# Kernel optimization log

Measured on AMD Instinct MI355X. Metric: run time of the kernel, lower is better.

The kernel has to match this reference:

```python
import jax, jax.numpy as jnp
import numpy as np

B, S, D, H, L = 32, 512, 512, 8, 6
NQ, FF, V, C = 8, 2048, 32000, 10
DK = D // H
EPS = 1e-5


def _layernorm(x, g, b):
    mu = jnp.mean(x, axis=-1, keepdims=True)
    var = jnp.mean(jnp.square(x - mu), axis=-1, keepdims=True)
    return (x - mu) * jax.lax.rsqrt(var + EPS) * g + b


def _pos_encoding(seq_len, dim):
    pos = jnp.arange(seq_len, dtype=jnp.float32)[:, None]
    div = jnp.exp(jnp.arange(0, dim, 2, dtype=jnp.float32) * (-jnp.log(10000.0) / dim))
    pe = jnp.zeros((seq_len, dim), dtype=jnp.float32)
    pe = pe.at[:, 0::2].set(jnp.sin(pos * div))
    pe = pe.at[:, 1::2].set(jnp.cos(pos * div))
    return pe


def setup_inputs() -> dict:
    key = jax.random.key(0)
    ks = jax.random.split(key, 16)
    sd = 0.02
    return {
        "x": jax.random.randint(ks[0], (B, S), 0, V),
        "emb": jax.random.normal(ks[1], (V, D), jnp.float32) * sd,
        "ln1_g": jnp.ones((L, D), jnp.float32),
        "ln1_b": jnp.zeros((L, D), jnp.float32),
        "ln2_g": jnp.ones((L, D), jnp.float32),
        "ln2_b": jnp.zeros((L, D), jnp.float32),
        "attn_w": jax.random.normal(ks[2], (L, D, D), jnp.float32) * sd,
        "attn_b": jnp.zeros((L, D), jnp.float32),
        "theta": jax.random.normal(ks[3], (L, NQ), jnp.float32),
        "ffn_w1": jax.random.normal(ks[4], (L, NQ, FF), jnp.float32) * sd,
        "ffn_b1": jnp.zeros((L, FF), jnp.float32),
        "ffn_w2": jax.random.normal(ks[5], (L, FF, D), jnp.float32) * sd,
        "ffn_b2": jnp.zeros((L, D), jnp.float32),
        "clf_w": jax.random.normal(ks[6], (D, C), jnp.float32) * sd,
        "clf_b": jnp.zeros((C,), jnp.float32),
    }


def reference(x, emb, ln1_g, ln1_b, ln2_g, ln2_b, attn_w, attn_b, theta,
              ffn_w1, ffn_b1, ffn_w2, ffn_b2, clf_w, clf_b):
    h = emb[x] + _pos_encoding(S, D)[None]  # [B,S,D]
    scale = 1.0 / jnp.sqrt(jnp.float32(DK))
    for l in range(L):
        # --- MultiHeadAttentionQuantum: q=k=v=reshape(x), no projections ---
        q = h.reshape(B, S, H, DK)
        scores = jnp.einsum('bihd,bjhd->bhij', q, q) * scale
        p = jax.nn.softmax(scores, axis=-1)
        attn = jnp.einsum('bhij,bjhd->bihd', p, q).reshape(B, S, D)
        attn = attn @ attn_w[l] + attn_b[l]
        h = _layernorm(h + attn, ln1_g[l], ln1_b[l])
        # --- FeedForwardQuantum: per-wire RX-encode -> RY(theta) -> <Z> = cos(x)cos(theta) ---
        qout = jnp.cos(h[..., :NQ]) * jnp.cos(theta[l])  # [B,S,NQ]
        f = jax.nn.relu(qout @ ffn_w1[l] + ffn_b1[l]) @ ffn_w2[l] + ffn_b2[l]
        h = _layernorm(h + f, ln2_g[l], ln2_b[l])
    pooled = jnp.mean(h, axis=1)  # [B,D]
    return pooled @ clf_w + clf_b  # [B,C]
```

## Files before the change

### kernel.cpp

```cpp
#include <hip/hip_runtime.h>
#include <hip/hip_bf16.h>
#include <math.h>

#define BB 32
#define SS 512
#define DD 512
#define HH 8
#define DK 64
#define LL 6
#define NQ 8
#define FF 2048
#define CC 10

typedef unsigned int uint;
typedef unsigned short ushort_t;
using bf16x8 = __attribute__((ext_vector_type(8))) short;
using f32x4  = __attribute__((ext_vector_type(4))) float;

#define MFMA(a, b, c) __builtin_amdgcn_mfma_f32_16x16x32_bf16((a), (b), (c), 0, 0, 0)

union U8 { ushort_t u[8]; bf16x8 v; };

__device__ __forceinline__ void gload16(const void* g, void* l) {
    __builtin_amdgcn_global_load_lds((__attribute__((address_space(1))) void*)g,
                                     (__attribute__((address_space(3))) void*)l,
                                     16, 0, 0);
}

__device__ inline ushort_t f2bf(float x) {
    uint u = __float_as_uint(x);
    u += 0x7FFFu + ((u >> 16) & 1u);
    return (ushort_t)(u >> 16);
}
__device__ inline void tsplit(float v, ushort_t& hi, ushort_t& lo) {
    uint u = __float_as_uint(v);
    hi = (ushort_t)(u >> 16);
    lo = f2bf(v - __uint_as_float(u & 0xFFFF0000u));
}
__device__ inline void tsplit_fast(float v, ushort_t& hi, ushort_t& lo) {
    uint u = __float_as_uint(v);
    hi = (ushort_t)(u >> 16);
    float res = v - __uint_as_float(u & 0xFFFF0000u);
    lo = (ushort_t)(__float_as_uint(res) >> 16);
}
__device__ inline uint packsplit(float v) {
    uint u = __float_as_uint(v) & 0xFFFF0000u;
    uint ru = __float_as_uint(v - __uint_as_float(u));
    ru += 0x7FFFu + ((ru >> 16) & 1u);
    return u | (ru >> 16);
}
__device__ inline float unpackf(uint u) {
    return __uint_as_float(u & 0xFFFF0000u) + __uint_as_float(u << 16);
}

__global__ __launch_bounds__(256) void embed_pe(const int* __restrict__ x,
                                                const float* __restrict__ emb,
                                                uint* __restrict__ Hp) {
    int idx = blockIdx.x * 256 + threadIdx.x;
    if (idx >= BB * SS * DD) return;
    int d = idx & (DD - 1);
    int s = (idx >> 9) & (SS - 1);
    int tok = x[idx >> 9];
    int i2 = d >> 1;
    float freq = expf((float)(2 * i2) * (-9.210340371976184f / (float)DD));
    float ang = (float)s * freq;
    float pe = (d & 1) ? cosf(ang) : sinf(ang);
    Hp[idx] = packsplit(emb[(size_t)tok * DD + d] + pe);
}

__global__ __launch_bounds__(256) void transpose_split_w(const float* __restrict__ in,
                                                         ushort_t* __restrict__ outh,
                                                         ushort_t* __restrict__ outl,
                                                         int K, int N) {
    __shared__ ushort_t th[64][68], tl[64][68];
    int nb = N >> 6;
    int k0 = ((int)blockIdx.x / nb) << 6;
    int n0 = ((int)blockIdx.x % nb) << 6;
    int t = threadIdx.x;
    int r = t >> 2, cb = (t & 3) << 4;
#pragma unroll
    for (int c = 0; c < 4; c++) {
        float4 v = *reinterpret_cast<const float4*>(&in[(size_t)(k0 + r) * N + n0 + cb + 4 * c]);
        float vv[4] = {v.x, v.y, v.z, v.w};
#pragma unroll
        for (int e = 0; e < 4; e++) {
            ushort_t hb, lb; tsplit(vv[e], hb, lb);
            th[r][cb + 4 * c + e] = hb;
            tl[r][cb + 4 * c + e] = lb;
        }
    }
    __syncthreads();
    int n = t >> 2, kb = (t & 3) << 4;
#pragma unroll
    for (int c = 0; c < 4; c++) {
        ushort4 oh, ol;
        oh.x = th[kb + 4 * c + 0][n]; ol.x = tl[kb + 4 * c + 0][n];
        oh.y = th[kb + 4 * c + 1][n]; ol.y = tl[kb + 4 * c + 1][n];
        oh.z = th[kb + 4 * c + 2][n]; ol.z = tl[kb + 4 * c + 2][n];
        oh.w = th[kb + 4 * c + 3][n]; ol.w = tl[kb + 4 * c + 3][n];
        *reinterpret_cast<ushort4*>(&outh[(size_t)(n0 + n) * K + k0 + kb + 4 * c]) = oh;
        *reinterpret_cast<ushort4*>(&outl[(size_t)(n0 + n) * K + k0 + kb + 4 * c]) = ol;
    }
}

__global__ __launch_bounds__(256) void prep_w1t(const float* __restrict__ W1all,
                                                ushort_t* __restrict__ outh,
                                                ushort_t* __restrict__ outl) {
    int l = blockIdx.y;
    int f = blockIdx.x * 256 + threadIdx.x;
    const float* W1 = W1all + (size_t)l * NQ * FF;
    U8 ph, pl;
#pragma unroll
    for (int n = 0; n < 8; n++) {
        ushort_t hb, lb; tsplit(W1[n * FF + f], hb, lb);
        ph.u[n] = hb; pl.u[n] = lb;
    }
    *reinterpret_cast<bf16x8*>(&outh[((size_t)l * FF + f) * 8]) = ph.v;
    *reinterpret_cast<bf16x8*>(&outl[((size_t)l * FF + f) * 8]) = pl.v;
}

__global__ __launch_bounds__(512, 4) void flash_attn_split(const uint* __restrict__ Hp,
                                                           ushort_t* __restrict__ outh,
                                                           ushort_t* __restrict__ outl) {
    __shared__ __align__(16) ushort_t Kh[64][72], Kl[64][72];
    __shared__ __align__(16) ushort_t Vh[64][72], Vl[64][72];
    __shared__ __align__(16) ushort_t Ph[128][72], Pl[128][72];

    int i0 = blockIdx.x * 128;
    int h0 = blockIdx.y * DK;
    int b  = blockIdx.z;
    const uint* baseH = Hp + (size_t)b * (SS * DD);

    int t = threadIdx.x;
    int w = t >> 6;
    int ln = t & 63;
    int l15 = ln & 15, lh = ln >> 4;

    bf16x8 aqh0, aqh1, aql0, aql1;
    {
        int row = i0 + w * 16 + l15;
        const uint* src = &baseH[(size_t)row * DD + h0 + lh * 8];
        uint4 p0 = *reinterpret_cast<const uint4*>(src);
        uint4 p1 = *reinterpret_cast<const uint4*>(src + 4);
        uint4 p2 = *reinterpret_cast<const uint4*>(src + 32);
        uint4 p3 = *reinterpret_cast<const uint4*>(src + 36);
        uint a0[8] = {p0.x, p0.y, p0.z, p0.w, p1.x, p1.y, p1.z, p1.w};
        uint a1[8] = {p2.x, p2.y, p2.z, p2.w, p3.x, p3.y, p3.z, p3.w};
        U8 h0u, l0u, h1u, l1u;
#pragma unroll
        for (int e = 0; e < 8; e++) {
            h0u.u[e] = (ushort_t)(a0[e] >> 16);
            l0u.u[e] = (ushort_t)(a0[e] & 0xFFFFu);
            h1u.u[e] = (ushort_t)(a1[e] >> 16);
            l1u.u[e] = (ushort_t)(a1[e] & 0xFFFFu);
        }
        aqh0 = h0u.v; aql0 = l0u.v; aqh1 = h1u.v; aql1 = l1u.v;
    }

    float m_[4], l_[4], al[4];
    f32x4 acc[4];
    f32x4 z4 = {0.f, 0.f, 0.f, 0.f};
#pragma unroll
    for (int r = 0; r < 4; r++) { m_[r] = -1e30f; l_[r] = 0.f; acc[r] = z4; }

    int kr = t >> 3, kcb = (t & 7) * 8;
    int vc = t & 7, vr = t >> 3;

    for (int j0 = 0; j0 < SS; j0 += 64) {
        __syncthreads();
        {
            const uint* src = &baseH[(size_t)(j0 + kr) * DD + h0 + kcb];
            uint4 p0 = *reinterpret_cast<const uint4*>(src);
            uint4 p1 = *reinterpret_cast<const uint4*>(src + 4);
            uint a[8] = {p0.x, p0.y, p0.z, p0.w, p1.x, p1.y, p1.z, p1.w};
            U8 kh, kl;
#pragma unroll
            for (int e = 0; e < 8; e++) {
                kh.u[e] = (ushort_t)(a[e] >> 16);
                kl.u[e] = (ushort_t)(a[e] & 0xFFFFu);
            }
            *reinterpret_cast<bf16x8*>(&Kh[kr][kcb]) = kh.v;
            *reinterpret_cast<bf16x8*>(&Kl[kr][kcb]) = kl.v;
        }
        __syncthreads();
#pragma unroll
        for (int e = 0; e < 8; e++) {
            int d = vc + 8 * e;
            Vh[d][vr] = Kh[vr][d];
            Vl[d][vr] = Kl[vr][d];
        }
        f32x4 sc[4];
#pragma unroll
        for (int tt = 0; tt < 4; tt++) {
            bf16x8 bh0 = *reinterpret_cast<const bf16x8*>(&Kh[tt * 16 + l15][lh * 8]);
            bf16x8 bh1 = *reinterpret_cast<const bf16x8*>(&Kh[tt * 16 + l15][32 + lh * 8]);
            bf16x8 bl0 = *reinterpret_cast<const bf16x8*>(&Kl[tt * 16 + l15][lh * 8]);
            bf16x8 bl1 = *reinterpret_cast<const bf16x8*>(&Kl[tt * 16 + l15][32 + lh * 8]);
            f32x4 s = z4;
            s = MFMA(aqh0, bh0, s);
            s = MFMA(aqh1, bh1, s);
            s = MFMA(aqh0, bl0, s);
            s = MFMA(aqh1, bl1, s);
            s = MFMA(aql0, bh0, s);
            s = MFMA(aql1, bh1, s);
            sc[tt] = s * 0.125f;
        }
#pragma unroll
        for (int r = 0; r < 4; r++) {
            float mx = fmaxf(fmaxf(sc[0][r], sc[1][r]), fmaxf(sc[2][r], sc[3][r]));
            mx = fmaxf(mx, __shfl_xor(mx, 1));
            mx = fmaxf(mx, __shfl_xor(mx, 2));
            mx = fmaxf(mx, __shfl_xor(mx, 4));
            mx = fmaxf(mx, __shfl_xor(mx, 8));
            float nm = fmaxf(m_[r], mx);
            al[r] = __expf(m_[r] - nm);
            m_[r] = nm;
            float rs = 0.f;
#pragma unroll
            for (int tt = 0; tt < 4; tt++) {
                float p = __expf(sc[tt][r] - nm);
                sc[tt][r] = p;
                rs += p;
            }
            rs += __shfl_xor(rs, 1);
            rs += __shfl_xor(rs, 2);
            rs += __shfl_xor(rs, 4);
            rs += __shfl_xor(rs, 8);
            l_[r] = l_[r] * al[r] + rs;
        }
#pragma unroll
        for (int tt = 0; tt < 4; tt++)
#pragma unroll
            for (int r = 0; r < 4; r++) {
                ushort_t hb, lb; tsplit(sc[tt][r], hb, lb);
                Ph[w * 16 + lh * 4 + r][tt * 16 + l15] = hb;
                Pl[w * 16 + lh * 4 + r][tt * 16 + l15] = lb;
            }
        __syncthreads();
#pragma unroll
        for (int td = 0; td < 4; td++) {
            acc[td][0] *= al[0];
            acc[td][1] *= al[1];
            acc[td][2] *= al[2];
            acc[td][3] *= al[3];
        }
        bf16x8 aph0 = *reinterpret_cast<const bf16x8*>(&Ph[w * 16 + l15][lh * 8]);
        bf16x8 aph1 = *reinterpret_cast<const bf16x8*>(&Ph[w * 16 + l15][32 + lh * 8]);
        bf16x8 apl0 = *reinterpret_cast<const bf16x8*>(&Pl[w * 16 + l15][lh * 8]);
        bf16x8 apl1 = *reinterpret_cast<const bf16x8*>(&Pl[w * 16 + l15][32 + lh * 8]);
#pragma unroll
        for (int td = 0; td < 4; td++) {
            bf16x8 bvh0 = *reinterpret_cast<const bf16x8*>(&Vh[td * 16 + l15][lh * 8]);
            bf16x8 bvh1 = *reinterpret_cast<const bf16x8*>(&Vh[td * 16 + l15][32 + lh * 8]);
            bf16x8 bvl0 = *reinterpret_cast<const bf16x8*>(&Vl[td * 16 + l15][lh * 8]);
            bf16x8 bvl1 = *reinterpret_cast<const bf16x8*>(&Vl[td * 16 + l15][32 + lh * 8]);
            acc[td] = MFMA(aph0, bvh0, acc[td]);
            acc[td] = MFMA(aph1, bvh1, acc[td]);
            acc[td] = MFMA(aph0, bvl0, acc[td]);
            acc[td] = MFMA(aph1, bvl1, acc[td]);
            acc[td] = MFMA(apl0, bvh0, acc[td]);
            acc[td] = MFMA(apl1, bvh1, acc[td]);
        }
    }

#pragma unroll
    for (int r = 0; r < 4; r++) {
        float inv = 1.f / l_[r];
        int row = i0 + w * 16 + lh * 4 + r;
#pragma unroll
        for (int td = 0; td < 4; td++) {
            float o = acc[td][r] * inv;
            ushort_t hb, lb; tsplit(o, hb, lb);
            size_t idx = (size_t)b * SS * DD + (size_t)row * DD + h0 + td * 16 + l15;
            outh[idx] = hb;
            outl[idx] = lb;
        }
    }
}

#define SWZREAD(plane, row, ks) \
    (*reinterpret_cast<const bf16x8*>(&(plane)[row][((((ks) * 4 + lh) ^ ((row) & 7)) * 8)]))

__global__ __launch_bounds__(512, 2) void gemm_split(const ushort_t* __restrict__ Ah,
                                                     const ushort_t* __restrict__ Al,
                                                     const ushort_t* __restrict__ Bth,
                                                     const ushort_t* __restrict__ Btl,
                                                     const float* __restrict__ bias,
                                                     float* __restrict__ C,
                                                     int M, int N, int K) {
    __shared__ __align__(16) ushort_t sAh[2][128][64], sAl[2][128][64];
    __shared__ __align__(16) ushort_t sBh[2][128][64], sBl[2][128][64];
    int nb = N >> 7;
    int m0 = ((int)blockIdx.x / nb) << 7;
    int n0 = ((int)blockIdx.x % nb) << 7;
    int t = threadIdx.x;
    int w = t >> 6, ln = t & 63, l15 = ln & 15, lh = ln >> 4;
    int wr = (w >> 2) * 64, wc = (w & 3) * 32;

    f32x4 z4 = {0.f, 0.f, 0.f, 0.f};
    f32x4 acc[4][2];
#pragma unroll
    for (int i = 0; i < 4; i++)
#pragma unroll
        for (int j = 0; j < 2; j++) acc[i][j] = z4;

    int srow = ln >> 3;
    int schunk = (ln & 7) ^ srow;

    auto stage = [&](int buf, int kk) {
#pragma unroll
        for (int p = 0; p < 2; p++) {
            int rbase = (w + p * 8) * 8;
            int grow = rbase + srow;
            int gc = kk + schunk * 8;
            gload16(&Ah[(size_t)(m0 + grow) * K + gc],  &sAh[buf][rbase][0]);
            gload16(&Al[(size_t)(m0 + grow) * K + gc],  &sAl[buf][rbase][0]);
            gload16(&Bth[(size_t)(n0 + grow) * K + gc], &sBh[buf][rbase][0]);
            gload16(&Btl[(size_t)(n0 + grow) * K + gc], &sBl[buf][rbase][0]);
        }
    };

    stage(0, 0);
    __syncthreads();
    int cur = 0;
    int ntile = K >> 6;

    for (int kt = 0; kt < ntile; kt++) {
        if (kt + 1 < ntile) stage(cur ^ 1, (kt + 1) * 64);
#pragma unroll
        for (int ks = 0; ks < 2; ks++) {
            bf16x8 ah[4], al_[4];
#pragma unroll
            for (int mt = 0; mt < 4; mt++) {
                int row = wr + mt * 16 + l15;
                ah[mt]  = SWZREAD(sAh[cur], row, ks);
                al_[mt] = SWZREAD(sAl[cur], row, ks);
            }
#pragma unroll
            for (int nt = 0; nt < 2; nt++) {
                int row = wc + nt * 16 + l15;
                bf16x8 bh = SWZREAD(sBh[cur], row, ks);
                bf16x8 bl = SWZREAD(sBl[cur], row, ks);
#pragma unroll
                for (int mt = 0; mt < 4; mt++) {
                    acc[mt][nt] = MFMA(ah[mt], bh, acc[mt][nt]);
                    acc[mt][nt] = MFMA(ah[mt], bl, acc[mt][nt]);
                    acc[mt][nt] = MFMA(al_[mt], bh, acc[mt][nt]);
                }
            }
        }
        __syncthreads();
        cur ^= 1;
    }
#pragma unroll
    for (int nt = 0; nt < 2; nt++) {
        int col = n0 + wc + nt * 16 + l15;
        float bs = bias[col];
#pragma unroll
        for (int mt = 0; mt < 4; mt++)
#pragma unroll
            for (int r = 0; r < 4; r++)
                C[(size_t)(m0 + wr + mt * 16 + lh * 4 + r) * N + col] = acc[mt][nt][r] + bs;
    }
}

__global__ __launch_bounds__(256) void ln_residual(uint* __restrict__ Hp,
                                                   const float* __restrict__ add,
                                                   const float* __restrict__ g,
                                                   const float* __restrict__ bta) {
    int row = blockIdx.x * 4 + (threadIdx.x >> 6);
    int lane = threadIdx.x & 63;
    uint* hp = Hp + (size_t)row * DD;
    const float* ap = add + (size_t)row * DD;
    float v[8];
    float sum = 0.f;
#pragma unroll
    for (int i = 0; i < 8; i++) {
        int d = lane + i * 64;
        v[i] = unpackf(hp[d]) + ap[d];
        sum += v[i];
    }
#pragma unroll
    for (int off = 32; off > 0; off >>= 1) sum += __shfl_xor(sum, off);
    float mu = sum * (1.f / DD);
    float s2 = 0.f;
#pragma unroll
    for (int i = 0; i < 8; i++) {
        float d2 = v[i] - mu;
        s2 += d2 * d2;
    }
#pragma unroll
    for (int off = 32; off > 0; off >>= 1) s2 += __shfl_xor(s2, off);
    float inv = rsqrtf(s2 * (1.f / DD) + 1e-5f);
#pragma unroll
    for (int i = 0; i < 8; i++) {
        int d = lane + i * 64;
        hp[d] = packsplit((v[i] - mu) * inv * g[d] + bta[d]);
    }
}

__global__ __launch_bounds__(512, 2) void ffn_split(const uint* __restrict__ Hp,
                                                    const ushort_t* __restrict__ W1th,
                                                    const ushort_t* __restrict__ W1tl,
                                                    const float* __restrict__ b1,
                                                    const ushort_t* __restrict__ W2th,
                                                    const ushort_t* __restrict__ W2tl,
                                                    const float* __restrict__ b2,
                                                    const float* __restrict__ theta,
                                                    float* __restrict__ outp) {
    __shared__ __align__(16) ushort_t Abh[128][72], Abl[128][72];
    __shared__ __align__(16) ushort_t sBh[2][128][64], sBl[2][128][64];
    __shared__ __align__(16) ushort_t qsh[129][8], qsl[129][8];
    __shared__ float tcs[8];

    int t = threadIdx.x;
    int m0 = (int)(blockIdx.x >> 2) * 128;
    int n0 = (int)(blockIdx.x & 3) * 128;
    if (t < 8) {
        tcs[t] = cosf(theta[t]);
        qsh[128][t] = 0;
        qsl[128][t] = 0;
    }
    __syncthreads();
#pragma unroll
    for (int i = 0; i < 2; i++) {
        int idx = t + i * 512;
        int m = idx >> 3, n = idx & 7;
        float q = cosf(unpackf(Hp[(size_t)(m0 + m) * DD + n])) * tcs[n];
        ushort_t hb, lb; tsplit(q, hb, lb);
        qsh[m][n] = hb;
        qsl[m][n] = lb;
    }

    int w = t >> 6, ln = t & 63, l15 = ln & 15, lh = ln >> 4;
    int wr = (w >> 2) * 64, wc = (w & 3) * 32;
    bool lh0 = (lh == 0);
    f32x4 z4 = {0.f, 0.f, 0.f, 0.f};
    bf16x8 z8 = {0, 0, 0, 0, 0, 0, 0, 0};
    f32x4 acc[4][2];
#pragma unroll
    for (int i = 0; i < 4; i++)
#pragma unroll
        for (int j = 0; j < 2; j++) acc[i][j] = z4;

    int srow = ln >> 3;
    int schunk = (ln & 7) ^ srow;

    auto stageB = [&](int buf, int kk) {
#pragma unroll
        for (int p = 0; p < 2; p++) {
            int rbase = (w + p * 8) * 8;
            int grow = rbase + srow;
            int gc = kk + schunk * 8;
            gload16(&W2th[(size_t)(n0 + grow) * FF + gc], &sBh[buf][rbase][0]);
            gload16(&W2tl[(size_t)(n0 + grow) * FF + gc], &sBl[buf][rbase][0]);
        }
    };

    bf16x8 rwh[4], rwl[4];
    stageB(0, 0);
#pragma unroll
    for (int fq = 0; fq < 4; fq++) {
        rwh[fq] = *reinterpret_cast<const bf16x8*>(&W1th[(size_t)(fq * 16 + l15) * 8]);
        rwl[fq] = *reinterpret_cast<const bf16x8*>(&W1tl[(size_t)(fq * 16 + l15) * 8]);
    }
    __syncthreads();
    int cur = 0;

    for (int k0 = 0; k0 < FF; k0 += 64) {
        {
            bf16x8 wh[4], wl[4];
#pragma unroll
            for (int fq = 0; fq < 4; fq++) {
                wh[fq] = lh0 ? rwh[fq] : z8;
                wl[fq] = lh0 ? rwl[fq] : z8;
            }
            int m = w * 16 + l15;
            int mrow = lh0 ? m : 128;
            bf16x8 qh  = *reinterpret_cast<const bf16x8*>(&qsh[mrow][0]);
            bf16x8 ql_ = *reinterpret_cast<const bf16x8*>(&qsl[mrow][0]);
#pragma unroll
            for (int fq = 0; fq < 4; fq++) {
                f32x4 d = z4;
                d = MFMA(wh[fq], qh, d);
                d = MFMA(wh[fq], ql_, d);
                d = MFMA(wl[fq], qh, d);
                float4 b1v = *reinterpret_cast<const float4*>(&b1[k0 + fq * 16 + lh * 4]);
                float v0 = fmaxf(d[0] + b1v.x, 0.f);
                float v1 = fmaxf(d[1] + b1v.y, 0.f);
                float v2 = fmaxf(d[2] + b1v.z, 0.f);
                float v3 = fmaxf(d[3] + b1v.w, 0.f);
                ushort_t h0_, l0_, h1_, l1_, h2_, l2_, h3_, l3_;
                tsplit_fast(v0, h0_, l0_);
                tsplit_fast(v1, h1_, l1_);
                tsplit_fast(v2, h2_, l2_);
                tsplit_fast(v3, h3_, l3_);
                uint2 hu, lu;
                hu.x = (uint)h0_ | ((uint)h1_ << 16);
                hu.y = (uint)h2_ | ((uint)h3_ << 16);
                lu.x = (uint)l0_ | ((uint)l1_ << 16);
                lu.y = (uint)l2_ | ((uint)l3_ << 16);
                *reinterpret_cast<uint2*>(&Abh[m][fq * 16 + lh * 4]) = hu;
                *reinterpret_cast<uint2*>(&Abl[m][fq * 16 + lh * 4]) = lu;
            }
        }
        __syncthreads();
        if (k0 + 64 < FF) {
            int k1 = k0 + 64;
            stageB(cur ^ 1, k1);
#pragma unroll
            for (int fq = 0; fq < 4; fq++) {
                rwh[fq] = *reinterpret_cast<const bf16x8*>(&W1th[(size_t)(k1 + fq * 16 + l15) * 8]);
                rwl[fq] = *reinterpret_cast<const bf16x8*>(&W1tl[(size_t)(k1 + fq * 16 + l15) * 8]);
            }
        }
#pragma unroll
        for (int ks = 0; ks < 2; ks++) {
            bf16x8 ah[4], al_[4];
#pragma unroll
            for (int mt = 0; mt < 4; mt++) {
                ah[mt]  = *reinterpret_cast<const bf16x8*>(&Abh[wr + mt * 16 + l15][ks * 32 + lh * 8]);
                al_[mt] = *reinterpret_cast<const bf16x8*>(&Abl[wr + mt * 16 + l15][ks * 32 + lh * 8]);
            }
#pragma unroll
            for (int nt = 0; nt < 2; nt++) {
                int row = wc + nt * 16 + l15;
                bf16x8 bh = SWZREAD(sBh[cur], row, ks);
                bf16x8 bl = SWZREAD(sBl[cur], row, ks);
#pragma unroll
                for (int mt = 0; mt < 4; mt++) {
                    acc[mt][nt] = MFMA(ah[mt], bh, acc[mt][nt]);
                    acc[mt][nt] = MFMA(ah[mt], bl, acc[mt][nt]);
                    acc[mt][nt] = MFMA(al_[mt], bh, acc[mt][nt]);
                }
            }
        }
        __syncthreads();
        cur ^= 1;
    }
#pragma unroll
    for (int nt = 0; nt < 2; nt++) {
        int col = n0 + wc + nt * 16 + l15;
        float bs = b2[col];
#pragma unroll
        for (int mt = 0; mt < 4; mt++)
#pragma unroll
            for (int r = 0; r < 4; r++)
                outp[(size_t)(m0 + wr + mt * 16 + lh * 4 + r) * DD + col] = acc[mt][nt][r] + bs;
    }
}

__global__ __launch_bounds__(256) void pool_mean(const uint* __restrict__ Hp,
                                                 float* __restrict__ pooled) {
    int idx = blockIdx.x * 256 + threadIdx.x;
    if (idx >= BB * DD) return;
    int b = idx >> 9, d = idx & 511;
    float s = 0.f;
    for (int j = 0; j < SS; j++) s += unpackf(Hp[((size_t)b * SS + j) * DD + d]);
    pooled[idx] = s * (1.f / SS);
}

__global__ __launch_bounds__(64) void classifier(const float* __restrict__ pooled,
                                                 const float* __restrict__ W,
                                                 const float* __restrict__ bias,
                                                 float* __restrict__ out) {
    int o = blockIdx.x;
    int b = o / CC, c = o % CC;
    int lane = threadIdx.x;
    float s = 0.f;
    for (int d = lane; d < DD; d += 64) s += pooled[b * DD + d] * W[d * CC + c];
#pragma unroll
    for (int off = 32; off > 0; off >>= 1) s += __shfl_xor(s, off);
    if (lane == 0) out[o] = s + bias[c];
}

extern "C" void kernel_launch(void* const* d_in, const int* in_sizes, int n_in,
                              void* d_out, int out_size, void* d_ws, size_t ws_size,
                              hipStream_t stream) {
    (void)in_sizes; (void)n_in; (void)out_size; (void)ws_size;
    const int*   x      = (const int*)d_in[0];
    const float* emb    = (const float*)d_in[1];
    const float* ln1_g  = (const float*)d_in[2];
    const float* ln1_b  = (const float*)d_in[3];
    const float* ln2_g  = (const float*)d_in[4];
    const float* ln2_b  = (const float*)d_in[5];
    const float* attn_w = (const float*)d_in[6];
    const float* attn_b = (const float*)d_in[7];
    const float* theta  = (const float*)d_in[8];
    const float* ffn_w1 = (const float*)d_in[9];
    const float* ffn_b1 = (const float*)d_in[10];
    const float* ffn_w2 = (const float*)d_in[11];
    const float* ffn_b2 = (const float*)d_in[12];
    const float* clf_w  = (const float*)d_in[13];
    const float* clf_b  = (const float*)d_in[14];
    float* out = (float*)d_out;

    char* ws = (char*)d_ws;
    uint*     Hp     = (uint*)(ws);
    float*    t2     = (float*)(ws + 33554432);
    ushort_t* t1h    = (ushort_t*)(ws + 67108864);
    ushort_t* t1l    = (ushort_t*)(ws + 83886080);
    float*    pooled = (float*)(ws + 100663296);
    ushort_t* Wath   = (ushort_t*)(ws + 100728832);
    ushort_t* Watl   = (ushort_t*)(ws + 101253120);
    ushort_t* W1th6  = (ushort_t*)(ws + 101777408);
    ushort_t* W1tl6  = (ushort_t*)(ws + 101974016);
    ushort_t* W2th   = (ushort_t*)(ws + 67108864);
    ushort_t* W2tl   = (ushort_t*)(ws + 67108864 + 2097152);

    embed_pe<<<(BB * SS * DD + 255) / 256, 256, 0, stream>>>(x, emb, Hp);
    prep_w1t<<<dim3(FF / 256, LL), 256, 0, stream>>>(ffn_w1, W1th6, W1tl6);

    for (int l = 0; l < LL; l++) {
        flash_attn_split<<<dim3(SS / 128, HH, BB), 512, 0, stream>>>(Hp, t1h, t1l);
        transpose_split_w<<<(DD / 64) * (DD / 64), 256, 0, stream>>>(
            attn_w + (size_t)l * DD * DD, Wath, Watl, DD, DD);
        gemm_split<<<(16384 / 128) * (DD / 128), 512, 0, stream>>>(
            t1h, t1l, Wath, Watl, attn_b + l * DD, t2, BB * SS, DD, DD);
        ln_residual<<<BB * SS / 4, 256, 0, stream>>>(Hp, t2, ln1_g + l * DD, ln1_b + l * DD);
        transpose_split_w<<<(FF / 64) * (DD / 64), 256, 0, stream>>>(
            ffn_w2 + (size_t)l * FF * DD, W2th, W2tl, FF, DD);
        ffn_split<<<(16384 / 128) * (DD / 128), 512, 0, stream>>>(
            Hp, W1th6 + (size_t)l * FF * 8, W1tl6 + (size_t)l * FF * 8, ffn_b1 + l * FF,
            W2th, W2tl, ffn_b2 + l * DD, theta + l * NQ, t2);
        ln_residual<<<BB * SS / 4, 256, 0, stream>>>(Hp, t2, ln2_g + l * DD, ln2_b + l * DD);
    }

    pool_mean<<<(BB * DD + 255) / 256, 256, 0, stream>>>(Hp, pooled);
    classifier<<<BB * CC, 64, 0, stream>>>(pooled, clf_w, clf_b, out);
}
```

Measured before the change: 1.994 ms.

## Single-buffer LDS tiles in GEMM and FFN kernels to raise occupancy

Both gemm_split and ffn_split drop the double-buffered LDS staging and use a single buffer with a sync before and after each load. Launch bounds are raised from 2 to 4 blocks per CU, trading software prefetch overlap for more resident waves to hide latency. LDS per block is halved (64KB to 32KB for gemm), but register pressure under the tighter bound may cause spills. Loads now sit on the critical path of each k-iteration.

New measurement: 1.941 ms. 1.03x faster.

```diff
diff --git a/kernel.cpp b/kernel.cpp
--- a/kernel.cpp
+++ b/kernel.cpp
@@ -281,15 +281,15 @@
 #define SWZREAD(plane, row, ks) \
     (*reinterpret_cast<const bf16x8*>(&(plane)[row][((((ks) * 4 + lh) ^ ((row) & 7)) * 8)]))
 
-__global__ __launch_bounds__(512, 2) void gemm_split(const ushort_t* __restrict__ Ah,
+__global__ __launch_bounds__(512, 4) void gemm_split(const ushort_t* __restrict__ Ah,
                                                      const ushort_t* __restrict__ Al,
                                                      const ushort_t* __restrict__ Bth,
                                                      const ushort_t* __restrict__ Btl,
                                                      const float* __restrict__ bias,
                                                      float* __restrict__ C,
                                                      int M, int N, int K) {
-    __shared__ __align__(16) ushort_t sAh[2][128][64], sAl[2][128][64];
-    __shared__ __align__(16) ushort_t sBh[2][128][64], sBl[2][128][64];
+    __shared__ __align__(16) ushort_t sAh[128][64], sAl[128][64];
+    __shared__ __align__(16) ushort_t sBh[128][64], sBl[128][64];
     int nb = N >> 7;
     int m0 = ((int)blockIdx.x / nb) << 7;
     int n0 = ((int)blockIdx.x % nb) << 7;
@@ -307,40 +307,35 @@
     int srow = ln >> 3;
     int schunk = (ln & 7) ^ srow;
 
-    auto stage = [&](int buf, int kk) {
+    int ntile = K >> 6;
+    for (int kt = 0; kt < ntile; kt++) {
+        __syncthreads();
+        int kk = kt * 64;
 #pragma unroll
         for (int p = 0; p < 2; p++) {
             int rbase = (w + p * 8) * 8;
             int grow = rbase + srow;
             int gc = kk + schunk * 8;
-            gload16(&Ah[(size_t)(m0 + grow) * K + gc],  &sAh[buf][rbase][0]);
-            gload16(&Al[(size_t)(m0 + grow) * K + gc],  &sAl[buf][rbase][0]);
-            gload16(&Bth[(size_t)(n0 + grow) * K + gc], &sBh[buf][rbase][0]);
-            gload16(&Btl[(size_t)(n0 + grow) * K + gc], &sBl[buf][rbase][0]);
-        }
-    };
-
-    stage(0, 0);
-    __syncthreads();
-    int cur = 0;
-    int ntile = K >> 6;
-
-    for (int kt = 0; kt < ntile; kt++) {
-        if (kt + 1 < ntile) stage(cur ^ 1, (kt + 1) * 64);
+            gload16(&Ah[(size_t)(m0 + grow) * K + gc],  &sAh[rbase][0]);
+            gload16(&Al[(size_t)(m0 + grow) * K + gc],  &sAl[rbase][0]);
+            gload16(&Bth[(size_t)(n0 + grow) * K + gc], &sBh[rbase][0]);
+            gload16(&Btl[(size_t)(n0 + grow) * K + gc], &sBl[rbase][0]);
+        }
+        __syncthreads();
 #pragma unroll
         for (int ks = 0; ks < 2; ks++) {
             bf16x8 ah[4], al_[4];
 #pragma unroll
             for (int mt = 0; mt < 4; mt++) {
                 int row = wr + mt * 16 + l15;
-                ah[mt]  = SWZREAD(sAh[cur], row, ks);
-                al_[mt] = SWZREAD(sAl[cur], row, ks);
+                ah[mt]  = SWZREAD(sAh, row, ks);
+                al_[mt] = SWZREAD(sAl, row, ks);
             }
 #pragma unroll
             for (int nt = 0; nt < 2; nt++) {
                 int row = wc + nt * 16 + l15;
-                bf16x8 bh = SWZREAD(sBh[cur], row, ks);
-                bf16x8 bl = SWZREAD(sBl[cur], row, ks);
+                bf16x8 bh = SWZREAD(sBh, row, ks);
+                bf16x8 bl = SWZREAD(sBl, row, ks);
 #pragma unroll
                 for (int mt = 0; mt < 4; mt++) {
                     acc[mt][nt] = MFMA(ah[mt], bh, acc[mt][nt]);
@@ -349,8 +344,6 @@
                 }
             }
         }
-        __syncthreads();
-        cur ^= 1;
     }
 #pragma unroll
     for (int nt = 0; nt < 2; nt++) {
@@ -399,7 +392,7 @@
     }
 }
 
-__global__ __launch_bounds__(512, 2) void ffn_split(const uint* __restrict__ Hp,
+__global__ __launch_bounds__(512, 4) void ffn_split(const uint* __restrict__ Hp,
                                                     const ushort_t* __restrict__ W1th,
                                                     const ushort_t* __restrict__ W1tl,
                                                     const float* __restrict__ b1,
@@ -409,7 +402,7 @@
                                                     const float* __restrict__ theta,
                                                     float* __restrict__ outp) {
     __shared__ __align__(16) ushort_t Abh[128][72], Abl[128][72];
-    __shared__ __align__(16) ushort_t sBh[2][128][64], sBl[2][128][64];
+    __shared__ __align__(16) ushort_t sBh[128][64], sBl[128][64];
     __shared__ __align__(16) ushort_t qsh[129][8], qsl[129][8];
     __shared__ float tcs[8];
 
@@ -446,28 +439,23 @@
     int srow = ln >> 3;
     int schunk = (ln & 7) ^ srow;
 
-    auto stageB = [&](int buf, int kk) {
+    bf16x8 rwh[4], rwl[4];
+#pragma unroll
+    for (int fq = 0; fq < 4; fq++) {
+        rwh[fq] = *reinterpret_cast<const bf16x8*>(&W1th[(size_t)(fq * 16 + l15) * 8]);
+        rwl[fq] = *reinterpret_cast<const bf16x8*>(&W1tl[(size_t)(fq * 16 + l15) * 8]);
+    }
+
+    for (int k0 = 0; k0 < FF; k0 += 64) {
+        __syncthreads();
 #pragma unroll
         for (int p = 0; p < 2; p++) {
             int rbase = (w + p * 8) * 8;
             int grow = rbase + srow;
-            int gc = kk + schunk * 8;
-            gload16(&W2th[(size_t)(n0 + grow) * FF + gc], &sBh[buf][rbase][0]);
-            gload16(&W2tl[(size_t)(n0 + grow) * FF + gc], &sBl[buf][rbase][0]);
-        }
-    };
-
-    bf16x8 rwh[4], rwl[4];
-    stageB(0, 0);
-#pragma unroll
-    for (int fq = 0; fq < 4; fq++) {
-        rwh[fq] = *reinterpret_cast<const bf16x8*>(&W1th[(size_t)(fq * 16 + l15) * 8]);
-        rwl[fq] = *reinterpret_cast<const bf16x8*>(&W1tl[(size_t)(fq * 16 + l15) * 8]);
-    }
-    __syncthreads();
-    int cur = 0;
-
-    for (int k0 = 0; k0 < FF; k0 += 64) {
+            int gc = k0 + schunk * 8;
+            gload16(&W2th[(size_t)(n0 + grow) * FF + gc], &sBh[rbase][0]);
+            gload16(&W2tl[(size_t)(n0 + grow) * FF + gc], &sBl[rbase][0]);
+        }
         {
             bf16x8 wh[4], wl[4];
 #pragma unroll
@@ -507,7 +495,6 @@
         __syncthreads();
         if (k0 + 64 < FF) {
             int k1 = k0 + 64;
-            stageB(cur ^ 1, k1);
 #pragma unroll
             for (int fq = 0; fq < 4; fq++) {
                 rwh[fq] = *reinterpret_cast<const bf16x8*>(&W1th[(size_t)(k1 + fq * 16 + l15) * 8]);
@@ -525,8 +512,8 @@
 #pragma unroll
             for (int nt = 0; nt < 2; nt++) {
                 int row = wc + nt * 16 + l15;
-                bf16x8 bh = SWZREAD(sBh[cur], row, ks);
-                bf16x8 bl = SWZREAD(sBl[cur], row, ks);
+                bf16x8 bh = SWZREAD(sBh, row, ks);
+                bf16x8 bl = SWZREAD(sBl, row, ks);
 #pragma unroll
                 for (int mt = 0; mt < 4; mt++) {
                     acc[mt][nt] = MFMA(ah[mt], bh, acc[mt][nt]);
@@ -535,8 +522,6 @@
                 }
             }
         }
-        __syncthreads();
-        cur ^= 1;
     }
 #pragma unroll
     for (int nt = 0; nt < 2; nt++) {
```
